# Optimization experiments

Hardware: AMD Instinct MI355X
Metric: run time of the kernel (lower is better)

## Reference

```python
import jax, jax.numpy as jnp
import numpy as np

K = 3  # involution kernel size


def dwconv3x3(x, w, b):
    # x: [B,C,H,W], w: [C,1,3,3] (depthwise, groups=C), b: [C]
    y = jax.lax.conv_general_dilated(
        x, w, window_strides=(1, 1), padding='SAME',
        dimension_numbers=('NCHW', 'OIHW', 'NCHW'),
        feature_group_count=x.shape[1])
    return y + b[None, :, None, None]


def conv1x1(x, w, b):
    # x: [B,C,H,W], w: [O,C], b: [O]
    return jnp.einsum('oc,bchw->bohw', w, x) + b[None, :, None, None]


def extract_patches(x):
    # x: [B,C,H,W] -> [B,C,K*K,H,W], zero-padded 'same' 3x3 neighborhoods
    B, C, H, W = x.shape
    p = (K - 1) // 2
    xp = jnp.pad(x, ((0, 0), (0, 0), (p, p), (p, p)))
    return jnp.stack([xp[:, :, i:i + H, j:j + W]
                      for i in range(K) for j in range(K)], axis=2)


def involution(x, w_red, b_red, w_span, b_span):
    # dynamic per-pixel kernels: [B, K*K, H, W]
    kern = conv1x1(jax.nn.relu(conv1x1(x, w_red, b_red)), w_span, b_span)
    patches = extract_patches(x)                 # [B,C,KK,H,W]
    return jnp.einsum('bkhw,bckhw->bchw', kern, patches)


def setup_inputs() -> dict:
    key = jax.random.key(0)
    ks = jax.random.split(key, 10)
    dim, red = 256, 64  # reduction ratio 4
    B, H, W = 8, 64, 64
    s = 0.05
    return {
        'x': jax.random.normal(ks[0], (B, dim, H, W), jnp.float32),
        'w_in': jax.random.normal(ks[1], (dim, 1, 3, 3), jnp.float32) * s,
        'b_in': jax.random.normal(ks[2], (dim,), jnp.float32) * s,
        'w_red': jax.random.normal(ks[3], (red, dim), jnp.float32) * s,
        'b_red': jax.random.normal(ks[4], (red,), jnp.float32) * s,
        'w_span': jax.random.normal(ks[5], (K * K, red), jnp.float32) * s,
        'b_span': jax.random.normal(ks[6], (K * K,), jnp.float32) * s,
        'w_out': jax.random.normal(ks[7], (dim, 1, 3, 3), jnp.float32) * s,
        'b_out': jax.random.normal(ks[8], (dim,), jnp.float32) * s,
    }


def reference(x, w_in, b_in, w_red, b_red, w_span, b_span, w_out, b_out):
    x = dwconv3x3(x, w_in, b_in)
    x = involution(x, w_red, b_red, w_span, b_span)
    x = dwconv3x3(x, w_out, b_out)
    return x
```

## Files before the change

### kernel.cpp

```cpp
#include <hip/hip_runtime.h>

#define BB 8
#define CC 256
#define HH 64
#define WW 64
#define RED 64
#define HW 4096
#define AST 72
#define LS 68

typedef __attribute__((ext_vector_type(8))) short s8v;
typedef __attribute__((ext_vector_type(4))) float f4v;

__device__ __forceinline__ unsigned short f2bf(float f) {
    unsigned u = __float_as_uint(f);
    u += 0x7fff + ((u >> 16) & 1);
    return (unsigned short)(u >> 16);
}

__global__ __launch_bounds__(256) void build_wtf(const float* __restrict__ w_red,
                                                 unsigned short* __restrict__ wtf) {
    int e = blockIdx.x * 256 + threadIdx.x;
    int j = e & 7, l = (e >> 3) & 63, nt = (e >> 9) & 3, kbg = e >> 11;
    int o = nt * 16 + (l & 15);
    int c = kbg * 32 + ((l >> 4) & 3) * 8 + j;
    wtf[e] = f2bf(w_red[o * CC + c]);
}

__global__ __launch_bounds__(512, 4) void dw_kern(const float* __restrict__ x,
                                                  const float* __restrict__ w_in,
                                                  const float* __restrict__ b_in,
                                                  const unsigned short* __restrict__ wtf,
                                                  const float* __restrict__ b_red,
                                                  const float* __restrict__ w_span,
                                                  const float* __restrict__ b_span,
                                                  float* __restrict__ kern) {
    alignas(16) __shared__ char smem[16640 + 18432];
    unsigned short* xs = (unsigned short*)smem;
    float* r_lds = (float*)smem;
    float* part  = (float*)(smem + 16640);

    const int t  = threadIdx.x;
    const int bx = blockIdx.x;
    const int h  = ((bx & 7) << 3) | (bx >> 3);
    const int b  = blockIdx.y;
    const int l  = t & 63;
    const int wv = t >> 6;
    const int mt = wv & 3, nh = wv >> 2;
    const int m0 = mt << 4;
    const int q  = t & 15;
    const int w0 = q << 2;
    const int cr = t >> 4;

    float4 pv[2][3]; float plf[2][3], prt[2][3];

    auto loadX = [&](int c0) {
        #pragma unroll
        for (int s = 0; s < 2; s++) {
            const int cc = c0 + s * 32 + cr;
            const float* xp = x + ((size_t)(b * CC + cc)) * HW;
            #pragma unroll
            for (int ky = 0; ky < 3; ky++) {
                int hh = h + ky - 1;
                if (hh < 0 || hh >= HH) {
                    pv[s][ky] = make_float4(0.f, 0.f, 0.f, 0.f);
                    plf[s][ky] = 0.f; prt[s][ky] = 0.f;
                    continue;
                }
                const float* row = xp + hh * WW + w0;
                pv[s][ky]  = *(const float4*)row;
                plf[s][ky] = (w0 > 0)      ? row[-1] : 0.f;
                prt[s][ky] = (w0 + 4 < WW) ? row[4]  : 0.f;
            }
        }
    };
    auto computeA = [&](int c0) {
        #pragma unroll
        for (int s = 0; s < 2; s++) {
            const int cl = s * 32 + cr;
            const int cc = c0 + cl;
            const float* wp = w_in + cc * 9;
            const float bb = b_in[cc];
            float4 a4 = make_float4(bb, bb, bb, bb);
            #pragma unroll
            for (int ky = 0; ky < 3; ky++) {
                float4 v = pv[s][ky];
                float lf = plf[s][ky], rt = prt[s][ky];
                float k0 = wp[ky * 3 + 0], k1 = wp[ky * 3 + 1], k2 = wp[ky * 3 + 2];
                a4.x = fmaf(k0, lf,  a4.x); a4.y = fmaf(k0, v.x, a4.y);
                a4.z = fmaf(k0, v.y, a4.z); a4.w = fmaf(k0, v.z, a4.w);
                a4.x = fmaf(k1, v.x, a4.x); a4.y = fmaf(k1, v.y, a4.y);
                a4.z = fmaf(k1, v.z, a4.z); a4.w = fmaf(k1, v.w, a4.w);
                a4.x = fmaf(k2, v.y, a4.x); a4.y = fmaf(k2, v.z, a4.y);
                a4.z = fmaf(k2, v.w, a4.z); a4.w = fmaf(k2, rt,  a4.w);
            }
            xs[(w0 + 0) * AST + cl] = f2bf(a4.x);
            xs[(w0 + 1) * AST + cl] = f2bf(a4.y);
            xs[(w0 + 2) * AST + cl] = f2bf(a4.z);
            xs[(w0 + 3) * AST + cl] = f2bf(a4.w);
        }
    };

    s8v bfr[2][2];
    auto loadB = [&](int k) {
        #pragma unroll
        for (int kb = 0; kb < 2; kb++)
            #pragma unroll
            for (int ntl = 0; ntl < 2; ntl++) {
                int nt = (nh << 1) + ntl;
                int kbg = (k << 1) + kb;
                bfr[kb][ntl] = *(const s8v*)(wtf + (((kbg * 4 + nt) * 64 + l) << 3));
            }
    };

    f4v acc[2] = {{0.f, 0.f, 0.f, 0.f}, {0.f, 0.f, 0.f, 0.f}};

    loadX(0); loadB(0);
    for (int k = 0; k < 4; k++) {
        computeA(k << 6);
        if (k < 3) loadX((k + 1) << 6);
        __syncthreads();
        #pragma unroll
        for (int kb = 0; kb < 2; kb++) {
            const unsigned short* ap =
                xs + (m0 + (l & 15)) * AST + (kb << 5) + ((l >> 4) & 3) * 8;
            s8v av = *(const s8v*)ap;
            #pragma unroll
            for (int ntl = 0; ntl < 2; ntl++)
                acc[ntl] = __builtin_amdgcn_mfma_f32_16x16x32_bf16(
                    av, bfr[kb][ntl], acc[ntl], 0, 0, 0);
        }
        if (k < 3) loadB(k + 1);
        __syncthreads();
    }

    #pragma unroll
    for (int ntl = 0; ntl < 2; ntl++) {
        int o = ((nh << 1) + ntl) * 16 + (l & 15);
        int pxr = m0 + ((l >> 4) & 3) * 4;
        #pragma unroll
        for (int i = 0; i < 4; i++)
            r_lds[o * 65 + pxr + i] = acc[ntl][i];
    }
    __syncthreads();

    const int px = t & 63;
    const int o0 = __builtin_amdgcn_readfirstlane(wv << 3);
    float kk[9];
    #pragma unroll
    for (int j = 0; j < 9; j++) kk[j] = 0.f;
    #pragma unroll
    for (int i = 0; i < 8; i++) {
        float r = fmaxf(r_lds[(o0 + i) * 65 + px] + b_red[o0 + i], 0.f);
        #pragma unroll
        for (int j = 0; j < 9; j++) kk[j] = fmaf(w_span[j * RED + o0 + i], r, kk[j]);
    }
    #pragma unroll
    for (int j = 0; j < 9; j++) part[(wv * 9 + j) * 64 + px] = kk[j];
    __syncthreads();
    if (wv == 0) {
        float* kp = kern + (size_t)b * 9 * HW + h * WW + px;
        #pragma unroll
        for (int j = 0; j < 9; j++) {
            float s = b_span[j];
            #pragma unroll
            for (int g = 0; g < 8; g++) s += part[(g * 9 + j) * 64 + px];
            kp[j * HW] = s;
        }
    }
}

__global__ __launch_bounds__(256) void invol_dw(const float* __restrict__ x,
                                                const float* __restrict__ w_in,
                                                const float* __restrict__ b_in,
                                                const float* __restrict__ kern,
                                                const float* __restrict__ w_out,
                                                const float* __restrict__ b_out,
                                                float* __restrict__ out) {
    __shared__ float xs[HH * LS];
    __shared__ float x1s[HH * LS];
    const int t  = threadIdx.x;
    const int q  = t & 15;
    const int w0 = q << 2;
    const int r  = t >> 4;
    const int c = blockIdx.x, b = blockIdx.y;
    const float* xp = x + ((size_t)(b * CC + c)) * HW;

    #pragma unroll
    for (int i = 0; i < 4; i++) {
        int h = r + (i << 4);
        *(float4*)&xs[h * LS + w0] = *(const float4*)(xp + h * WW + w0);
    }
    __syncthreads();

    {
        const float* wp = w_in + c * 9;
        const float bb = b_in[c];
        #pragma unroll
        for (int i = 0; i < 4; i++) {
            int h = r + (i << 4);
            float4 acc = make_float4(bb, bb, bb, bb);
            #pragma unroll
            for (int ky = 0; ky < 3; ky++) {
                int hh = h + ky - 1;
                if (hh < 0 || hh >= HH) continue;
                const float* row = &xs[hh * LS + w0];
                float4 v = *(const float4*)row;
                float lf = (w0 > 0)      ? row[-1] : 0.f;
                float rt = (w0 + 4 < WW) ? row[4]  : 0.f;
                float k0 = wp[ky * 3 + 0], k1 = wp[ky * 3 + 1], k2 = wp[ky * 3 + 2];
                acc.x = fmaf(k0, lf,  acc.x); acc.y = fmaf(k0, v.x, acc.y);
                acc.z = fmaf(k0, v.y, acc.z); acc.w = fmaf(k0, v.z, acc.w);
                acc.x = fmaf(k1, v.x, acc.x); acc.y = fmaf(k1, v.y, acc.y);
                acc.z = fmaf(k1, v.z, acc.z); acc.w = fmaf(k1, v.w, acc.w);
                acc.x = fmaf(k2, v.y, acc.x); acc.y = fmaf(k2, v.z, acc.y);
                acc.z = fmaf(k2, v.w, acc.z); acc.w = fmaf(k2, rt,  acc.w);
            }
            *(float4*)&x1s[h * LS + w0] = acc;
        }
    }
    __syncthreads();

    const float* kp = kern + (size_t)b * 9 * HW;
    #pragma unroll
    for (int i = 0; i < 4; i++) {
        int h  = r + (i << 4);
        int hw = h * WW + w0;
        float4 acc = make_float4(0.f, 0.f, 0.f, 0.f);
        #pragma unroll
        for (int ky = 0; ky < 3; ky++) {
            int hh = h + ky - 1;
            if (hh < 0 || hh >= HH) continue;
            const float* row = &x1s[hh * LS + w0];
            float4 v = *(const float4*)row;
            float lf = (w0 > 0)      ? row[-1] : 0.f;
            float rt = (w0 + 4 < WW) ? row[4]  : 0.f;
            float4 k0 = *(const float4*)(kp + (ky * 3 + 0) * HW + hw);
            float4 k1 = *(const float4*)(kp + (ky * 3 + 1) * HW + hw);
            float4 k2 = *(const float4*)(kp + (ky * 3 + 2) * HW + hw);
            acc.x = fmaf(k0.x, lf,  acc.x); acc.y = fmaf(k0.y, v.x, acc.y);
            acc.z = fmaf(k0.z, v.y, acc.z); acc.w = fmaf(k0.w, v.z, acc.w);
            acc.x = fmaf(k1.x, v.x, acc.x); acc.y = fmaf(k1.y, v.y, acc.y);
            acc.z = fmaf(k1.z, v.z, acc.z); acc.w = fmaf(k1.w, v.w, acc.w);
            acc.x = fmaf(k2.x, v.y, acc.x); acc.y = fmaf(k2.y, v.z, acc.y);
            acc.z = fmaf(k2.z, v.w, acc.z); acc.w = fmaf(k2.w, rt,  acc.w);
        }
        *(float4*)&xs[h * LS + w0] = acc;
    }
    __syncthreads();

    const float* wp = w_out + c * 9;
    const float bb = b_out[c];
    float* op = out + ((size_t)(b * CC + c)) * HW;
    #pragma unroll
    for (int i = 0; i < 4; i++) {
        int h = r + (i << 4);
        float4 acc = make_float4(bb, bb, bb, bb);
        #pragma unroll
        for (int ky = 0; ky < 3; ky++) {
            int hh = h + ky - 1;
            if (hh < 0 || hh >= HH) continue;
            const float* row = &xs[hh * LS + w0];
            float4 v = *(const float4*)row;
            float lf = (w0 > 0)      ? row[-1] : 0.f;
            float rt = (w0 + 4 < WW) ? row[4]  : 0.f;
            float k0 = wp[ky * 3 + 0], k1 = wp[ky * 3 + 1], k2 = wp[ky * 3 + 2];
            acc.x = fmaf(k0, lf,  acc.x); acc.y = fmaf(k0, v.x, acc.y);
            acc.z = fmaf(k0, v.y, acc.z); acc.w = fmaf(k0, v.z, acc.w);
            acc.x = fmaf(k1, v.x, acc.x); acc.y = fmaf(k1, v.y, acc.y);
            acc.z = fmaf(k1, v.z, acc.z); acc.w = fmaf(k1, v.w, acc.w);
            acc.x = fmaf(k2, v.y, acc.x); acc.y = fmaf(k2, v.z, acc.y);
            acc.z = fmaf(k2, v.w, acc.z); acc.w = fmaf(k2, rt,  acc.w);
        }
        *(float4*)(op + h * WW + w0) = acc;
    }
}

extern "C" void kernel_launch(void* const* d_in, const int* in_sizes, int n_in,
                              void* d_out, int out_size, void* d_ws, size_t ws_size,
                              hipStream_t stream) {
    const float* x      = (const float*)d_in[0];
    const float* w_in   = (const float*)d_in[1];
    const float* b_in   = (const float*)d_in[2];
    const float* w_red  = (const float*)d_in[3];
    const float* b_red  = (const float*)d_in[4];
    const float* w_span = (const float*)d_in[5];
    const float* b_span = (const float*)d_in[6];
    const float* w_out  = (const float*)d_in[7];
    const float* b_out  = (const float*)d_in[8];
    float* out = (float*)d_out;

    float* kern = (float*)d_ws;
    unsigned short* wtf = (unsigned short*)(kern + (size_t)BB * 9 * HW);

    build_wtf<<<64, 256, 0, stream>>>(w_red, wtf);
    dw_kern<<<dim3(HH, BB), 512, 0, stream>>>(x, w_in, b_in, wtf, b_red,
                                              w_span, b_span, kern);
    invol_dw<<<dim3(CC, BB), 256, 0, stream>>>(x, w_in, b_in, kern,
                                               w_out, b_out, out);
}
```

Measured before the change: 138.8 us.

## Store bf16 first-conv output for reuse and fold weight packing into GEMM kernel

The first kernel now writes its depthwise-conv output (already rounded to bf16 for the MFMA GEMM) to a global buffer. The involution kernel loads that buffer instead of re-reading fp32 x and recomputing the first depthwise conv. The separate weight-packing kernel is removed, and w_red is converted to bf16 fragments inline inside the GEMM kernel. This saves one launch and the duplicated conv work, and halves the bytes read by the second kernel, but adds a 16MB global write in the first kernel. It also lowers the involution input from fp32 to bf16, which costs some accuracy.

```diff
diff --git a/kernel.cpp b/kernel.cpp
--- a/kernel.cpp
+++ b/kernel.cpp
@@ -7,7 +7,8 @@
 #define RED 64
 #define HW 4096
 #define AST 72
-#define LS 68
+#define LSF 68
+#define LSH 72
 
 typedef __attribute__((ext_vector_type(8))) short s8v;
 typedef __attribute__((ext_vector_type(4))) float f4v;
@@ -17,24 +18,19 @@
     u += 0x7fff + ((u >> 16) & 1);
     return (unsigned short)(u >> 16);
 }
-
-__global__ __launch_bounds__(256) void build_wtf(const float* __restrict__ w_red,
-                                                 unsigned short* __restrict__ wtf) {
-    int e = blockIdx.x * 256 + threadIdx.x;
-    int j = e & 7, l = (e >> 3) & 63, nt = (e >> 9) & 3, kbg = e >> 11;
-    int o = nt * 16 + (l & 15);
-    int c = kbg * 32 + ((l >> 4) & 3) * 8 + j;
-    wtf[e] = f2bf(w_red[o * CC + c]);
+__device__ __forceinline__ float b2f(unsigned short u) {
+    return __uint_as_float(((unsigned)u) << 16);
 }
 
 __global__ __launch_bounds__(512, 4) void dw_kern(const float* __restrict__ x,
                                                   const float* __restrict__ w_in,
                                                   const float* __restrict__ b_in,
-                                                  const unsigned short* __restrict__ wtf,
+                                                  const float* __restrict__ w_red,
                                                   const float* __restrict__ b_red,
                                                   const float* __restrict__ w_span,
                                                   const float* __restrict__ b_span,
-                                                  float* __restrict__ kern) {
+                                                  float* __restrict__ kern,
+                                                  unsigned short* __restrict__ x1g) {
     alignas(16) __shared__ char smem[16640 + 18432];
     unsigned short* xs = (unsigned short*)smem;
     float* r_lds = (float*)smem;
@@ -94,10 +90,14 @@
                 a4.x = fmaf(k2, v.y, a4.x); a4.y = fmaf(k2, v.z, a4.y);
                 a4.z = fmaf(k2, v.w, a4.z); a4.w = fmaf(k2, rt,  a4.w);
             }
-            xs[(w0 + 0) * AST + cl] = f2bf(a4.x);
-            xs[(w0 + 1) * AST + cl] = f2bf(a4.y);
-            xs[(w0 + 2) * AST + cl] = f2bf(a4.z);
-            xs[(w0 + 3) * AST + cl] = f2bf(a4.w);
+            ushort4 pk;
+            pk.x = f2bf(a4.x); pk.y = f2bf(a4.y);
+            pk.z = f2bf(a4.z); pk.w = f2bf(a4.w);
+            xs[(w0 + 0) * AST + cl] = pk.x;
+            xs[(w0 + 1) * AST + cl] = pk.y;
+            xs[(w0 + 2) * AST + cl] = pk.z;
+            xs[(w0 + 3) * AST + cl] = pk.w;
+            *(ushort4*)(x1g + ((size_t)(b * CC + cc)) * HW + h * WW + w0) = pk;
         }
     };
 
@@ -107,9 +107,17 @@
         for (int kb = 0; kb < 2; kb++)
             #pragma unroll
             for (int ntl = 0; ntl < 2; ntl++) {
-                int nt = (nh << 1) + ntl;
-                int kbg = (k << 1) + kb;
-                bfr[kb][ntl] = *(const s8v*)(wtf + (((kbg * 4 + nt) * 64 + l) << 3));
+                const int o   = (((nh << 1) + ntl) << 4) + (l & 15);
+                const int c0b = (((k << 1) + kb) << 5) + ((l >> 4) & 3) * 8;
+                const float* wr = w_red + o * CC + c0b;
+                float4 f0 = *(const float4*)wr;
+                float4 f1 = *(const float4*)(wr + 4);
+                s8v bv;
+                bv[0] = (short)f2bf(f0.x); bv[1] = (short)f2bf(f0.y);
+                bv[2] = (short)f2bf(f0.z); bv[3] = (short)f2bf(f0.w);
+                bv[4] = (short)f2bf(f1.x); bv[5] = (short)f2bf(f1.y);
+                bv[6] = (short)f2bf(f1.z); bv[7] = (short)f2bf(f1.w);
+                bfr[kb][ntl] = bv;
             }
     };
 
@@ -170,54 +178,25 @@
     }
 }
 
-__global__ __launch_bounds__(256) void invol_dw(const float* __restrict__ x,
-                                                const float* __restrict__ w_in,
-                                                const float* __restrict__ b_in,
+__global__ __launch_bounds__(256) void invol_dw(const unsigned short* __restrict__ x1g,
                                                 const float* __restrict__ kern,
                                                 const float* __restrict__ w_out,
                                                 const float* __restrict__ b_out,
                                                 float* __restrict__ out) {
-    __shared__ float xs[HH * LS];
-    __shared__ float x1s[HH * LS];
+    __shared__ unsigned short x1s[HH * LSH];
+    __shared__ float res[HH * LSF];
     const int t  = threadIdx.x;
     const int q  = t & 15;
     const int w0 = q << 2;
     const int r  = t >> 4;
     const int c = blockIdx.x, b = blockIdx.y;
-    const float* xp = x + ((size_t)(b * CC + c)) * HW;
-
-    #pragma unroll
-    for (int i = 0; i < 4; i++) {
-        int h = r + (i << 4);
-        *(float4*)&xs[h * LS + w0] = *(const float4*)(xp + h * WW + w0);
-    }
-    __syncthreads();
 
     {
-        const float* wp = w_in + c * 9;
-        const float bb = b_in[c];
-        #pragma unroll
-        for (int i = 0; i < 4; i++) {
-            int h = r + (i << 4);
-            float4 acc = make_float4(bb, bb, bb, bb);
-            #pragma unroll
-            for (int ky = 0; ky < 3; ky++) {
-                int hh = h + ky - 1;
-                if (hh < 0 || hh >= HH) continue;
-                const float* row = &xs[hh * LS + w0];
-                float4 v = *(const float4*)row;
-                float lf = (w0 > 0)      ? row[-1] : 0.f;
-                float rt = (w0 + 4 < WW) ? row[4]  : 0.f;
-                float k0 = wp[ky * 3 + 0], k1 = wp[ky * 3 + 1], k2 = wp[ky * 3 + 2];
-                acc.x = fmaf(k0, lf,  acc.x); acc.y = fmaf(k0, v.x, acc.y);
-                acc.z = fmaf(k0, v.y, acc.z); acc.w = fmaf(k0, v.z, acc.w);
-                acc.x = fmaf(k1, v.x, acc.x); acc.y = fmaf(k1, v.y, acc.y);
-                acc.z = fmaf(k1, v.z, acc.z); acc.w = fmaf(k1, v.w, acc.w);
-                acc.x = fmaf(k2, v.y, acc.x); acc.y = fmaf(k2, v.z, acc.y);
-                acc.z = fmaf(k2, v.w, acc.z); acc.w = fmaf(k2, rt,  acc.w);
-            }
-            *(float4*)&x1s[h * LS + w0] = acc;
-        }
+        const unsigned short* xp = x1g + ((size_t)(b * CC + c)) * HW;
+        const int hl = t >> 2;
+        const int wl = (t & 3) << 4;
+        *(s8v*)&x1s[hl * LSH + wl]     = *(const s8v*)(xp + hl * WW + wl);
+        *(s8v*)&x1s[hl * LSH + wl + 8] = *(const s8v*)(xp + hl * WW + wl + 8);
     }
     __syncthreads();
 
@@ -231,21 +210,22 @@
         for (int ky = 0; ky < 3; ky++) {
             int hh = h + ky - 1;
             if (hh < 0 || hh >= HH) continue;
-            const float* row = &x1s[hh * LS + w0];
-            float4 v = *(const float4*)row;
-            float lf = (w0 > 0)      ? row[-1] : 0.f;
-            float rt = (w0 + 4 < WW) ? row[4]  : 0.f;
+            const unsigned short* row = &x1s[hh * LSH + w0];
+            float vx = b2f(row[0]), vy = b2f(row[1]);
+            float vz = b2f(row[2]), vw = b2f(row[3]);
+            float lf = (w0 > 0)      ? b2f(row[-1]) : 0.f;
+            float rt = (w0 + 4 < WW) ? b2f(row[4])  : 0.f;
             float4 k0 = *(const float4*)(kp + (ky * 3 + 0) * HW + hw);
             float4 k1 = *(const float4*)(kp + (ky * 3 + 1) * HW + hw);
             float4 k2 = *(const float4*)(kp + (ky * 3 + 2) * HW + hw);
-            acc.x = fmaf(k0.x, lf,  acc.x); acc.y = fmaf(k0.y, v.x, acc.y);
-            acc.z = fmaf(k0.z, v.y, acc.z); acc.w = fmaf(k0.w, v.z, acc.w);
-            acc.x = fmaf(k1.x, v.x, acc.x); acc.y = fmaf(k1.y, v.y, acc.y);
-            acc.z = fmaf(k1.z, v.z, acc.z); acc.w = fmaf(k1.w, v.w, acc.w);
-            acc.x = fmaf(k2.x, v.y, acc.x); acc.y = fmaf(k2.y, v.z, acc.y);
-            acc.z = fmaf(k2.z, v.w, acc.z); acc.w = fmaf(k2.w, rt,  acc.w);
-        }
-        *(float4*)&xs[h * LS + w0] = acc;
+            acc.x = fmaf(k0.x, lf, acc.x); acc.y = fmaf(k0.y, vx, acc.y);
+            acc.z = fmaf(k0.z, vy, acc.z); acc.w = fmaf(k0.w, vz, acc.w);
+            acc.x = fmaf(k1.x, vx, acc.x); acc.y = fmaf(k1.y, vy, acc.y);
+            acc.z = fmaf(k1.z, vz, acc.z); acc.w = fmaf(k1.w, vw, acc.w);
+            acc.x = fmaf(k2.x, vy, acc.x); acc.y = fmaf(k2.y, vz, acc.y);
+            acc.z = fmaf(k2.z, vw, acc.z); acc.w = fmaf(k2.w, rt, acc.w);
+        }
+        *(float4*)&res[h * LSF + w0] = acc;
     }
     __syncthreads();
 
@@ -260,7 +240,7 @@
         for (int ky = 0; ky < 3; ky++) {
             int hh = h + ky - 1;
             if (hh < 0 || hh >= HH) continue;
-            const float* row = &xs[hh * LS + w0];
+            const float* row = &res[hh * LSF + w0];
             float4 v = *(const float4*)row;
             float lf = (w0 > 0)      ? row[-1] : 0.f;
             float rt = (w0 + 4 < WW) ? row[4]  : 0.f;
@@ -291,11 +271,9 @@
     float* out = (float*)d_out;
 
     float* kern = (float*)d_ws;
-    unsigned short* wtf = (unsigned short*)(kern + (size_t)BB * 9 * HW);
-
-    build_wtf<<<64, 256, 0, stream>>>(w_red, wtf);
-    dw_kern<<<dim3(HH, BB), 512, 0, stream>>>(x, w_in, b_in, wtf, b_red,
-                                              w_span, b_span, kern);
-    invol_dw<<<dim3(CC, BB), 256, 0, stream>>>(x, w_in, b_in, kern,
-                                               w_out, b_out, out);
-}
+    unsigned short* x1g = (unsigned short*)(kern + (size_t)BB * 9 * HW);
+
+    dw_kern<<<dim3(HH, BB), 512, 0, stream>>>(x, w_in, b_in, w_red, b_red,
+                                              w_span, b_span, kern, x1g);
+    invol_dw<<<dim3(CC, BB), 256, 0, stream>>>(x1g, kern, w_out, b_out, out);
+}
```

Result: slower. 155.6 us (+12.1%).
